# Kernel optimization log

Hardware: AMD Instinct MI355X
Metric: run time of the kernel (lower is better)

Reference implementation:

```python
import jax, jax.numpy as jnp
import numpy as np

B, D, E, K = 32768, 512, 64, 4
NCTX = 16
H = (NCTX // 2 - 1) * 768  # 5376: per-expert context block, (n_ctx/2 - 1) rows of ctx_dim=768
NOISE_EPS = 1e-2
LOSS_COEF = 1e-2


def setup_inputs() -> dict:
    key = jax.random.key(0)
    ks = jax.random.split(key, 5)
    x = jax.random.normal(ks[0], (B, D), jnp.float32)
    w_gate = jax.random.normal(ks[1], (D, E), jnp.float32) * 0.02
    w_noise = jax.random.normal(ks[2], (D, E), jnp.float32) * 0.02
    noise = jax.random.normal(ks[3], (B, E), jnp.float32)
    ctx_c = jax.random.normal(ks[4], (E, H), jnp.float32) * 0.02
    return {"x": x, "w_gate": w_gate, "w_noise": w_noise, "noise": noise, "ctx_c": ctx_c}


def _cv_squared(v, eps=1e-10):
    # coefficient-of-variation squared: var / mean^2
    return jnp.var(v) / (jnp.mean(v) ** 2 + eps)


def _normal_cdf(z):
    return 0.5 * (1.0 + jax.lax.erf(z * (1.0 / np.sqrt(2.0))))


def reference(x, w_gate, w_noise, noise, ctx_c):
    # ---- noisy top-k gating (Shazeer sparsely-gated MoE) ----
    clean_logits = x @ w_gate                                    # [B, E]
    noise_stddev = jax.nn.softplus(x @ w_noise) + NOISE_EPS      # [B, E]
    noisy_logits = clean_logits + noise * noise_stddev           # [B, E]

    top_logits, top_idx = jax.lax.top_k(noisy_logits, K + 1)     # [B, K+1]
    top_k_logits = top_logits[:, :K]
    top_k_idx = top_idx[:, :K]
    top_k_gates = jax.nn.softmax(top_k_logits, axis=-1)          # [B, K]

    rows = jnp.arange(B)[:, None]
    gates = jnp.zeros((B, E), x.dtype).at[rows, top_k_idx].set(top_k_gates)  # sparse -> dense scatter

    # ---- load-balancing aux loss ----
    importance = gates.sum(axis=0)                               # [E]
    thr_in = top_logits[:, K][:, None]                           # (K+1)-th largest noisy logit
    thr_out = top_logits[:, K - 1][:, None]                      # K-th largest noisy logit
    is_in = noisy_logits > thr_in
    prob_in = _normal_cdf((clean_logits - thr_in) / noise_stddev)
    prob_out = _normal_cdf((clean_logits - thr_out) / noise_stddev)
    load = jnp.where(is_in, prob_in, prob_out).sum(axis=0)       # [E]
    aux_loss = (_cv_squared(importance) + _cv_squared(load)) * LOSS_COEF

    # ---- weighted combine of per-expert context vectors (as in LPromptLearner) ----
    out = jnp.einsum('be,eh->bh', gates, ctx_c)                  # [B, H]
    return out, aux_loss
```

## Files before the change

kernel.cpp:

```cpp
#include <hip/hip_runtime.h>
#include <math.h>

#define B_ 32768
#define D_ 512
#define E_ 64
#define H_ 5376
#define H4_ (H_ / 4)

typedef float f32x4 __attribute__((ext_vector_type(4)));
typedef _Float16 f16x8 __attribute__((ext_vector_type(8)));
typedef unsigned int u32x4 __attribute__((ext_vector_type(4)));

__device__ __forceinline__ unsigned short f16bits(_Float16 h) {
    union { _Float16 h; unsigned short u; } c; c.h = h; return c.u;
}

__global__ __launch_bounds__(256) void prep_kernel(
    const float* __restrict__ wgate, const float* __restrict__ wnoise,
    _Float16* __restrict__ wt0, _Float16* __restrict__ wt1)
{
    int e = blockIdx.x;
    const float* src = (e < E_) ? (wgate + e) : (wnoise + (e - E_));
    for (int k = threadIdx.x; k < D_; k += 256) {
        float v = src[(size_t)k * E_] * 1024.0f;
        _Float16 h0 = (_Float16)v;
        _Float16 h1 = (_Float16)(v - (float)h0);
        wt0[(size_t)e * D_ + k] = h0;
        wt1[(size_t)e * D_ + k] = h1;
    }
}

__global__ __launch_bounds__(256) void gate_kernel(
    const float* __restrict__ x,
    const _Float16* __restrict__ wt0,
    const _Float16* __restrict__ wt1,
    const float* __restrict__ noise,
    unsigned int* __restrict__ o_idx,
    float4* __restrict__ o_g,
    float* __restrict__ g_imp,
    float* __restrict__ g_load)
{
    __shared__ __align__(16) _Float16 x0s[64 * 128];
    __shared__ __align__(16) _Float16 x1s[64 * 128];
    __shared__ float s_imp[E_];
    __shared__ float s_load[E_];

    const int t  = threadIdx.x;
    const int w  = t >> 6;
    const int l  = t & 63;
    const int le = l & 15;
    const int g  = l >> 4;
    const int b0 = blockIdx.x * 64;

    if (t < E_) { s_imp[t] = 0.0f; s_load[t] = 0.0f; }

    f32x4 accAC[8], accB[8];
#pragma unroll
    for (int n = 0; n < 8; ++n) {
        accAC[n] = (f32x4){0.f, 0.f, 0.f, 0.f};
        accB[n]  = (f32x4){0.f, 0.f, 0.f, 0.f};
    }

    const int arow = w * 16 + le;
    for (int q = 0; q < 4; ++q) {
        __syncthreads();
#pragma unroll
        for (int i = 0; i < 4; ++i) {
            int id  = t + 256 * i;
            int row = id >> 4;
            int c   = id & 15;
            const float* src = x + (size_t)(b0 + row) * D_ + q * 128 + c * 8;
            float4 v0 = *(const float4*)src;
            float4 v1 = *(const float4*)(src + 4);
            float vv[8] = {v0.x, v0.y, v0.z, v0.w, v1.x, v1.y, v1.z, v1.w};
            unsigned int hw[4], lw[4];
#pragma unroll
            for (int p = 0; p < 4; ++p) {
                float va = vv[2*p] * 16.0f, vb = vv[2*p+1] * 16.0f;
                _Float16 a0 = (_Float16)va, b0f = (_Float16)vb;
                _Float16 a1 = (_Float16)((va - (float)a0) * 4096.0f);
                _Float16 b1 = (_Float16)((vb - (float)b0f) * 4096.0f);
                hw[p] = (unsigned)f16bits(a0) | ((unsigned)f16bits(b0f) << 16);
                lw[p] = (unsigned)f16bits(a1) | ((unsigned)f16bits(b1) << 16);
            }
            int addr = (row * 256 + c * 16) ^ ((row & 7) << 4);
            *(u32x4*)((char*)x0s + addr) = (u32x4){hw[0], hw[1], hw[2], hw[3]};
            *(u32x4*)((char*)x1s + addr) = (u32x4){lw[0], lw[1], lw[2], lw[3]};
        }
        __syncthreads();
#pragma unroll
        for (int s = 0; s < 4; ++s) {
            int aoff = (arow * 256 + s * 64 + g * 16) ^ ((arow & 7) << 4);
            f16x8 a0 = *(const f16x8*)((const char*)x0s + aoff);
            f16x8 a1 = *(const f16x8*)((const char*)x1s + aoff);
            int ks = q * 4 + s;
#pragma unroll
            for (int n = 0; n < 8; ++n) {
                size_t boff = (size_t)(n * 16 + le) * D_ + ks * 32 + g * 8;
                f16x8 b0 = *(const f16x8*)(wt0 + boff);
                f16x8 b1 = *(const f16x8*)(wt1 + boff);
                accAC[n] = __builtin_amdgcn_mfma_f32_16x16x32_f16(a0, b0, accAC[n], 0, 0, 0);
                accAC[n] = __builtin_amdgcn_mfma_f32_16x16x32_f16(a0, b1, accAC[n], 0, 0, 0);
                accB[n]  = __builtin_amdgcn_mfma_f32_16x16x32_f16(a1, b0, accB[n],  0, 0, 0);
            }
        }
    }

    const double UNSCALE = 1.0 / 16384.0;
    const double RESC    = 1.0 / 4096.0;
    float loadacc[4] = {0.f, 0.f, 0.f, 0.f};
#pragma unroll
    for (int r = 0; r < 4; ++r) {
        int li = w * 16 + g * 4 + r;
        int b  = b0 + li;
        double cl[4], sd[4], ny[4];
#pragma unroll
        for (int n = 0; n < 4; ++n) {
            cl[n] = ((double)accAC[n][r] + (double)accB[n][r] * RESC) * UNSCALE;
            double z = ((double)accAC[n+4][r] + (double)accB[n+4][r] * RESC) * UNSCALE;
            double sp = (z > 30.0) ? z : log1p(exp(z));
            sd[n] = sp + 0.01;
            float nz = noise[(size_t)b * E_ + le + 16 * n];
            ny[n] = cl[n] + (double)nz * sd[n];
        }
        double v[4] = {ny[0], ny[1], ny[2], ny[3]};
        double topv[5]; int topi[5];
#pragma unroll 1
        for (int s5 = 0; s5 < 5; ++s5) {
            double bm = v[0]; int bj = 0;
#pragma unroll
            for (int n = 1; n < 4; ++n) if (v[n] > bm) { bm = v[n]; bj = n; }
            int be = bj * 16 + le;
#pragma unroll
            for (int off = 1; off < 16; off <<= 1) {
                double om = __shfl_xor(bm, off, 64);
                int    oe = __shfl_xor(be, off, 64);
                if (om > bm || (om == bm && oe < be)) { bm = om; be = oe; }
            }
            topv[s5] = bm; topi[s5] = be;
            if ((be & 15) == le) v[be >> 4] = -1.0e300;
        }
        double m0 = topv[0];
        double e0 = exp(topv[0] - m0), e1 = exp(topv[1] - m0),
               e2 = exp(topv[2] - m0), e3 = exp(topv[3] - m0);
        double inv = 1.0 / (e0 + e1 + e2 + e3);
        float g0 = (float)(e0 * inv), g1 = (float)(e1 * inv),
              g2 = (float)(e2 * inv), g3 = (float)(e3 * inv);
        if (le == 0) {
            o_idx[b] = (unsigned)topi[0] | ((unsigned)topi[1] << 8) |
                       ((unsigned)topi[2] << 16) | ((unsigned)topi[3] << 24);
            float4 gv; gv.x = g0; gv.y = g1; gv.z = g2; gv.w = g3;
            o_g[b] = gv;
            atomicAdd(&s_imp[topi[0]], g0);
            atomicAdd(&s_imp[topi[1]], g1);
            atomicAdd(&s_imp[topi[2]], g2);
            atomicAdd(&s_imp[topi[3]], g3);
        }
        double thr_out = topv[3];
        double thr_in  = topv[4];
#pragma unroll
        for (int n = 0; n < 4; ++n) {
            double thr = (ny[n] > thr_in) ? thr_in : thr_out;
            float  zz  = (float)((cl[n] - thr) / sd[n]);
            loadacc[n] += 0.5f * (1.0f + erff(zz * 0.70710678118654752f));
        }
    }
#pragma unroll
    for (int n = 0; n < 4; ++n) atomicAdd(&s_load[16 * n + le], loadacc[n]);
    __syncthreads();
    if (t < E_) {
        atomicAdd(&g_imp[t],  s_imp[t]);
        atomicAdd(&g_load[t], s_load[t]);
    }
}

__global__ __launch_bounds__(256) void dispatch_kernel(
    const float* __restrict__ ctx,
    const unsigned int* __restrict__ o_idx,
    const float4* __restrict__ o_g,
    float* __restrict__ out)
{
    const int t = threadIdx.x;
    const int tb0 = blockIdx.x * 8;
#pragma unroll 1
    for (int s = 0; s < 8; s += 2) {
        int ba = tb0 + s, bb = ba + 1;
        unsigned pka = o_idx[ba], pkb = o_idx[bb];
        float4 ga = o_g[ba], gb = o_g[bb];
        const f32x4* a0 = (const f32x4*)&ctx[(size_t)(pka & 255u) * H_];
        const f32x4* a1 = (const f32x4*)&ctx[(size_t)((pka >> 8) & 255u) * H_];
        const f32x4* a2 = (const f32x4*)&ctx[(size_t)((pka >> 16) & 255u) * H_];
        const f32x4* a3 = (const f32x4*)&ctx[(size_t)(pka >> 24) * H_];
        const f32x4* c0 = (const f32x4*)&ctx[(size_t)(pkb & 255u) * H_];
        const f32x4* c1 = (const f32x4*)&ctx[(size_t)((pkb >> 8) & 255u) * H_];
        const f32x4* c2 = (const f32x4*)&ctx[(size_t)((pkb >> 16) & 255u) * H_];
        const f32x4* c3 = (const f32x4*)&ctx[(size_t)(pkb >> 24) * H_];
        f32x4* oa = (f32x4*)&out[(size_t)ba * H_];
        f32x4* ob = (f32x4*)&out[(size_t)bb * H_];
        for (int f = t; f < H4_; f += 256) {
            f32x4 ra = ga.x * a0[f] + ga.y * a1[f] + ga.z * a2[f] + ga.w * a3[f];
            f32x4 rb = gb.x * c0[f] + gb.y * c1[f] + gb.z * c2[f] + gb.w * c3[f];
            __builtin_nontemporal_store(ra, &oa[f]);
            __builtin_nontemporal_store(rb, &ob[f]);
        }
    }
}

__global__ void loss_kernel(const float* __restrict__ g_imp,
                            const float* __restrict__ g_load,
                            float* __restrict__ out)
{
    int e = threadIdx.x;
    double vi = (double)g_imp[e];
    double vl = (double)g_load[e];
    double si = vi, sl = vl;
#pragma unroll
    for (int off = 1; off < 64; off <<= 1) {
        si += __shfl_xor(si, off, 64);
        sl += __shfl_xor(sl, off, 64);
    }
    double mi = si / 64.0, ml = sl / 64.0;
    double di = vi - mi, dl = vl - ml;
    double qi = di * di, ql = dl * dl;
#pragma unroll
    for (int off = 1; off < 64; off <<= 1) {
        qi += __shfl_xor(qi, off, 64);
        ql += __shfl_xor(ql, off, 64);
    }
    double vari = qi / 64.0, varl = ql / 64.0;
    double cv2i = vari / (mi * mi + 1e-10);
    double cv2l = varl / (ml * ml + 1e-10);
    if (e == 0) out[(size_t)B_ * H_] = (float)((cv2i + cv2l) * 0.01);
}

extern "C" void kernel_launch(void* const* d_in, const int* in_sizes, int n_in,
                              void* d_out, int out_size, void* d_ws, size_t ws_size,
                              hipStream_t stream)
{
    const float* x      = (const float*)d_in[0];
    const float* wgate  = (const float*)d_in[1];
    const float* wnoise = (const float*)d_in[2];
    const float* noise  = (const float*)d_in[3];
    const float* ctx    = (const float*)d_in[4];
    float* out    = (float*)d_out;
    float* g_imp  = (float*)d_ws;
    float* g_load = g_imp + E_;
    _Float16* wt0 = (_Float16*)(g_load + E_);
    _Float16* wt1 = wt0 + 128 * D_;
    unsigned int* o_idx = (unsigned int*)(wt1 + 128 * D_);
    float4* o_g = (float4*)(o_idx + B_);

    (void)hipMemsetAsync(d_ws, 0, 2 * E_ * sizeof(float), stream);
    prep_kernel<<<128, 256, 0, stream>>>(wgate, wnoise, wt0, wt1);
    gate_kernel<<<B_ / 64, 256, 0, stream>>>(x, wt0, wt1, noise,
                                             o_idx, o_g, g_imp, g_load);
    dispatch_kernel<<<B_ / 8, 256, 0, stream>>>(ctx, o_idx, o_g, out);
    loss_kernel<<<1, 64, 0, stream>>>(g_imp, g_load, out);
}
```

Measured before the change: 243.2 us.

## Tile dispatch over H chunks and stage expert context slices in LDS

```diff
diff --git a/kernel.cpp b/kernel.cpp
--- a/kernel.cpp
+++ b/kernel.cpp
@@ -6,6 +6,8 @@
 #define E_ 64
 #define H_ 5376
 #define H4_ (H_ / 4)
+#define HC_ 128
+#define NCH_ (H_ / HC_)
 
 typedef float f32x4 __attribute__((ext_vector_type(4)));
 typedef _Float16 f16x8 __attribute__((ext_vector_type(8)));
@@ -180,29 +182,32 @@
     const float4* __restrict__ o_g,
     float* __restrict__ out)
 {
-    const int t = threadIdx.x;
-    const int tb0 = blockIdx.x * 8;
-#pragma unroll 1
-    for (int s = 0; s < 8; s += 2) {
-        int ba = tb0 + s, bb = ba + 1;
-        unsigned pka = o_idx[ba], pkb = o_idx[bb];
-        float4 ga = o_g[ba], gb = o_g[bb];
-        const f32x4* a0 = (const f32x4*)&ctx[(size_t)(pka & 255u) * H_];
-        const f32x4* a1 = (const f32x4*)&ctx[(size_t)((pka >> 8) & 255u) * H_];
-        const f32x4* a2 = (const f32x4*)&ctx[(size_t)((pka >> 16) & 255u) * H_];
-        const f32x4* a3 = (const f32x4*)&ctx[(size_t)(pka >> 24) * H_];
-        const f32x4* c0 = (const f32x4*)&ctx[(size_t)(pkb & 255u) * H_];
-        const f32x4* c1 = (const f32x4*)&ctx[(size_t)((pkb >> 8) & 255u) * H_];
-        const f32x4* c2 = (const f32x4*)&ctx[(size_t)((pkb >> 16) & 255u) * H_];
-        const f32x4* c3 = (const f32x4*)&ctx[(size_t)(pkb >> 24) * H_];
-        f32x4* oa = (f32x4*)&out[(size_t)ba * H_];
-        f32x4* ob = (f32x4*)&out[(size_t)bb * H_];
-        for (int f = t; f < H4_; f += 256) {
-            f32x4 ra = ga.x * a0[f] + ga.y * a1[f] + ga.z * a2[f] + ga.w * a3[f];
-            f32x4 rb = gb.x * c0[f] + gb.y * c1[f] + gb.z * c2[f] + gb.w * c3[f];
-            __builtin_nontemporal_store(ra, &oa[f]);
-            __builtin_nontemporal_store(rb, &ob[f]);
-        }
+    __shared__ f32x4 cs[E_ * (HC_ / 4)];
+
+    const int t  = threadIdx.x;
+    const int h0 = blockIdx.x * HC_;
+    const int tb = blockIdx.y * 64;
+
+#pragma unroll
+    for (int i = 0; i < 8; ++i) {
+        int idx = t + 256 * i;
+        int e = idx >> 5, c = idx & 31;
+        cs[idx] = *(const f32x4*)&ctx[(size_t)e * H_ + h0 + c * 4];
+    }
+    __syncthreads();
+
+    const int tok = t >> 5;
+    const int c   = t & 31;
+#pragma unroll
+    for (int s = 0; s < 8; ++s) {
+        int b = tb + s * 8 + tok;
+        unsigned pk = o_idx[b];
+        float4 g = o_g[b];
+        f32x4 r = g.x * cs[((pk      ) & 255u) * 32 + c]
+                + g.y * cs[((pk >>  8) & 255u) * 32 + c]
+                + g.z * cs[((pk >> 16) & 255u) * 32 + c]
+                + g.w * cs[( pk >> 24         ) * 32 + c];
+        __builtin_nontemporal_store(r, (f32x4*)&out[(size_t)b * H_ + h0 + c * 4]);
     }
 }
 
@@ -254,6 +259,6 @@
     prep_kernel<<<128, 256, 0, stream>>>(wgate, wnoise, wt0, wt1);
     gate_kernel<<<B_ / 64, 256, 0, stream>>>(x, wt0, wt1, noise,
                                              o_idx, o_g, g_imp, g_load);
-    dispatch_kernel<<<B_ / 8, 256, 0, stream>>>(ctx, o_idx, o_g, out);
+    dispatch_kernel<<<dim3(NCH_, B_ / 64), 256, 0, stream>>>(ctx, o_idx, o_g, out);
     loss_kernel<<<1, 64, 0, stream>>>(g_imp, g_load, out);
 }
```

Result: no change. 242.7 us (-0.2%).
